# Performance work log

Measured on AMD Instinct MI355X. Metric: run time of the kernel, lower is better.

The kernel has to match this reference:

```python
import jax, jax.numpy as jnp
import numpy as np
import itertools

MAX_SRC_PER_MIX = 2
N_OUT = 2 * MAX_SRC_PER_MIX          # 4 estimated sources
N_COMB = 2 ** N_OUT                  # 16 assignment combinations
SNR_MAX = 30.0


def _a_tensor():
    # [16, 2, 4]: row 0 = combination mask, row 1 = its complement
    combos = np.array(list(itertools.product([0, 1], repeat=N_OUT)), dtype=np.float32)
    return jnp.asarray(np.stack([combos, 1.0 - combos], axis=1))


def setup_inputs() -> dict:
    key = jax.random.key(0)
    k1, k2, k3 = jax.random.split(key, 3)
    B, T = 32, 64000
    return {
        "estimated_sources": jax.random.normal(k1, (B, N_OUT, T), dtype=jnp.float32),
        "m1": jax.random.normal(k2, (B, T), dtype=jnp.float32),
        "m2": jax.random.normal(k3, (B, T), dtype=jnp.float32),
    }


def _snr_loss(y, y_pred):
    # y: [K, B, T] estimated mixture, y_pred: [1, B, T] reference mixture
    a = jnp.sum((y - y_pred) ** 2, axis=-1)   # [K, B]
    b = jnp.sum(y ** 2, axis=-1)              # [K, B]
    loss = 10.0 * jnp.log10(a + SNR_MAX * b) - 10.0 * jnp.log10(b)
    return jnp.sum(loss, axis=-1)             # [K]


def reference(estimated_sources, m1, m2):
    A = _a_tensor()                                              # [K, 2, S]
    # all combinations x batch in one contraction (contraction dim S=4)
    mix = jnp.einsum('kcs,bst->kbct', A, estimated_sources)      # [K, B, 2, T]
    losses = _snr_loss(mix[:, :, 0], m1[None]) + _snr_loss(mix[:, :, 1], m2[None])  # [K]
    return jnp.argmin(losses), jnp.min(losses)
```

## Files before the change

### kernel.cpp

```cpp
#include <hip/hip_runtime.h>
#include <math.h>

#define B      32
#define NSRC   4
#define T      64000
#define CH     64
#define NACC   20
#define KCOMB  16
#define NBLK   (B * CH)
#define TLEN4  ((T / CH) / 4)

#define DPP_QX1   0xB1
#define DPP_QX2   0x4E
#define DPP_HMIRR 0x141
#define DPP_MIRR  0x140

template <int CTRL>
__device__ __forceinline__ float dpp_add(float v) {
    int x = __builtin_amdgcn_update_dpp(0, __float_as_int(v), CTRL, 0xF, 0xF, true);
    return v + __int_as_float(x);
}

__device__ __forceinline__ void accum20(float* __restrict__ acc,
        const float4 v0, const float4 v1, const float4 v2, const float4 v3,
        const float4 w1, const float4 w2)
{
    const float A0[4] = {v0.x, v0.y, v0.z, v0.w};
    const float A1[4] = {v1.x, v1.y, v1.z, v1.w};
    const float A2[4] = {v2.x, v2.y, v2.z, v2.w};
    const float A3[4] = {v3.x, v3.y, v3.z, v3.w};
    const float M1[4] = {w1.x, w1.y, w1.z, w1.w};
    const float M2[4] = {w2.x, w2.y, w2.z, w2.w};
#pragma unroll
    for (int j = 0; j < 4; j++) {
        float s0 = A0[j], s1 = A1[j], s2 = A2[j], s3 = A3[j];
        float x = M1[j], y = M2[j];
        acc[0]  = fmaf(s0, s0, acc[0]);
        acc[1]  = fmaf(s0, s1, acc[1]);
        acc[2]  = fmaf(s0, s2, acc[2]);
        acc[3]  = fmaf(s0, s3, acc[3]);
        acc[4]  = fmaf(s1, s1, acc[4]);
        acc[5]  = fmaf(s1, s2, acc[5]);
        acc[6]  = fmaf(s1, s3, acc[6]);
        acc[7]  = fmaf(s2, s2, acc[7]);
        acc[8]  = fmaf(s2, s3, acc[8]);
        acc[9]  = fmaf(s3, s3, acc[9]);
        acc[10] = fmaf(s0, x,  acc[10]);
        acc[11] = fmaf(s1, x,  acc[11]);
        acc[12] = fmaf(s2, x,  acc[12]);
        acc[13] = fmaf(s3, x,  acc[13]);
        acc[14] = fmaf(s0, y,  acc[14]);
        acc[15] = fmaf(s1, y,  acc[15]);
        acc[16] = fmaf(s2, y,  acc[16]);
        acc[17] = fmaf(s3, y,  acc[17]);
        acc[18] = fmaf(x,  x,  acc[18]);
        acc[19] = fmaf(y,  y,  acc[19]);
    }
}

__global__ __launch_bounds__(256) void mixit_reduce_kernel(
    const float* __restrict__ est, const float* __restrict__ m1,
    const float* __restrict__ m2, float* __restrict__ ws)
{
    const int tid = threadIdx.x;
    const int b   = blockIdx.x / CH;
    const int ch  = blockIdx.x % CH;

    const float4* e0 = (const float4*)(est + (size_t)b * NSRC * T) + (size_t)ch * TLEN4;
    const float4* e1 = e0 + T / 4;
    const float4* e2 = e1 + T / 4;
    const float4* e3 = e2 + T / 4;
    const float4* p1 = (const float4*)(m1 + (size_t)b * T) + (size_t)ch * TLEN4;
    const float4* p2 = (const float4*)(m2 + (size_t)b * T) + (size_t)ch * TLEN4;

    float acc[NACC];
#pragma unroll
    for (int i = 0; i < NACC; i++) acc[i] = 0.0f;

    if (tid < TLEN4) {
        float4 v0 = e0[tid], v1 = e1[tid], v2 = e2[tid], v3 = e3[tid];
        float4 w1 = p1[tid], w2 = p2[tid];
        accum20(acc, v0, v1, v2, v3, w1, w2);
    }

#pragma unroll
    for (int a = 0; a < NACC; a++) {
        float v = acc[a];
        v = dpp_add<DPP_QX1>(v);
        v = dpp_add<DPP_QX2>(v);
        v = dpp_add<DPP_HMIRR>(v);
        v = dpp_add<DPP_MIRR>(v);
        int x = __builtin_amdgcn_ds_swizzle(__float_as_int(v), 0x401F);
        acc[a] = v + __int_as_float(x);
    }

    const int lane = tid & 63;
    const int wave = tid >> 6;
    __shared__ float red[8][NACC];
    if (lane == 0 || lane == 32) {
        const int r = wave * 2 + (lane >> 5);
#pragma unroll
        for (int a = 0; a < NACC; a++) red[r][a] = acc[a];
    }
    __syncthreads();
    if (tid < NACC) {
        float s = 0.0f;
#pragma unroll
        for (int r = 0; r < 8; r++) s += red[r][tid];
        ws[(size_t)tid * NBLK + blockIdx.x] = s;
    }
}

__global__ __launch_bounds__(1024) void mixit_finalize_kernel(
    const float* __restrict__ ws, float* __restrict__ out)
{
    __shared__ float sums[B * NACC];
    __shared__ float lkb[KCOMB * B];
    __shared__ float losses[KCOMB];

    const int t = threadIdx.x;

    if (t < B * NACC) {
        const int a  = t >> 5;
        const int bb = t & 31;
        const float4* p = (const float4*)(ws + (size_t)a * NBLK + bb * CH);
        float4 s4 = p[0];
#pragma unroll
        for (int i = 1; i < CH / 4; i++) {
            float4 q = p[i];
            s4.x += q.x; s4.y += q.y; s4.z += q.z; s4.w += q.w;
        }
        sums[bb * NACC + a] = (s4.x + s4.y) + (s4.z + s4.w);
    }
    __syncthreads();

    if (t < KCOMB * B) {
        const int k  = t >> 5;
        const int bb = t & 31;
        const float k0 = (float)((k >> 3) & 1);
        const float k1 = (float)((k >> 2) & 1);
        const float k2 = (float)((k >> 1) & 1);
        const float k3 = (float)(k & 1);
        const float u0 = 1.0f - k0, u1 = 1.0f - k1, u2 = 1.0f - k2, u3 = 1.0f - k3;

        const float* a = sums + bb * NACC;
        float g00 = a[0], g01 = a[1], g02 = a[2], g03 = a[3];
        float g11 = a[4], g12 = a[5], g13 = a[6];
        float g22 = a[7], g23 = a[8], g33 = a[9];

        float q0 = k0*k0*g00 + k1*k1*g11 + k2*k2*g22 + k3*k3*g33
                 + 2.0f*(k0*k1*g01 + k0*k2*g02 + k0*k3*g03
                       + k1*k2*g12 + k1*k3*g13 + k2*k3*g23);
        float q1 = u0*u0*g00 + u1*u1*g11 + u2*u2*g22 + u3*u3*g33
                 + 2.0f*(u0*u1*g01 + u0*u2*g02 + u0*u3*g03
                       + u1*u2*g12 + u1*u3*g13 + u2*u3*g23);
        float d1 = k0*a[10] + k1*a[11] + k2*a[12] + k3*a[13];
        float d2 = u0*a[14] + u1*a[15] + u2*a[16] + u3*a[17];

        float a0 = q0 - 2.0f*d1 + a[18];
        float a1 = q1 - 2.0f*d2 + a[19];

        float l = 10.0f * (log10f(fmaf(30.0f, q0, a0)) - log10f(q0))
                + 10.0f * (log10f(fmaf(30.0f, q1, a1)) - log10f(q1));
        lkb[k * B + bb] = l;
    }
    __syncthreads();

    if (t < KCOMB) {
        float s = 0.0f;
#pragma unroll
        for (int bb = 0; bb < B; bb++) s += lkb[t * B + bb];
        losses[t] = s;
    }
    __syncthreads();

    if (t == 0) {
        float best = losses[0];
        int bi = 0;
        for (int k = 1; k < KCOMB; k++)
            if (losses[k] < best) { best = losses[k]; bi = k; }
        out[0] = (float)bi;
        out[1] = best;
    }
}

extern "C" void kernel_launch(void* const* d_in, const int* in_sizes, int n_in,
                              void* d_out, int out_size, void* d_ws, size_t ws_size,
                              hipStream_t stream) {
    const float* est = (const float*)d_in[0];
    const float* m1  = (const float*)d_in[1];
    const float* m2  = (const float*)d_in[2];
    float* ws  = (float*)d_ws;
    float* out = (float*)d_out;

    mixit_reduce_kernel<<<NBLK, 256, 0, stream>>>(est, m1, m2, ws);
    mixit_finalize_kernel<<<1, 1024, 0, stream>>>(ws, out);
}
```

Baseline: 91.69 us.

## Fuse reduce and finalize into one kernel using atomics and last-block detection

Merges the two-kernel pipeline into a single launch. Each block atomically adds its 20 partial sums into a per-batch accumulator, and a global counter picks the last block to run the finalize (loss per combination plus argmin). This removes the second kernel launch and the strided workspace reread, at the cost of a memset before each call, 20 atomics per block, and a serialized tail in one block. Memory ordering relies on relaxed atomics with no explicit fence before the counter increment, so correctness depends on the hardware ordering those operations.

```diff
diff --git a/kernel.cpp b/kernel.cpp
--- a/kernel.cpp
+++ b/kernel.cpp
@@ -9,6 +9,8 @@
 #define KCOMB  16
 #define NBLK   (B * CH)
 #define TLEN4  ((T / CH) / 4)
+
+#define CNT_FLOAT_OFF 1024
 
 #define DPP_QX1   0xB1
 #define DPP_QX2   0x4E
@@ -58,9 +60,10 @@
     }
 }
 
-__global__ __launch_bounds__(256) void mixit_reduce_kernel(
+__global__ __launch_bounds__(256) void mixit_onekernel(
     const float* __restrict__ est, const float* __restrict__ m1,
-    const float* __restrict__ m2, float* __restrict__ ws)
+    const float* __restrict__ m2, float* __restrict__ ws,
+    float* __restrict__ out)
 {
     const int tid = threadIdx.x;
     const int b   = blockIdx.x / CH;
@@ -103,40 +106,39 @@
         for (int a = 0; a < NACC; a++) red[r][a] = acc[a];
     }
     __syncthreads();
+
     if (tid < NACC) {
         float s = 0.0f;
 #pragma unroll
         for (int r = 0; r < 8; r++) s += red[r][tid];
-        ws[(size_t)tid * NBLK + blockIdx.x] = s;
-    }
-}
-
-__global__ __launch_bounds__(1024) void mixit_finalize_kernel(
-    const float* __restrict__ ws, float* __restrict__ out)
-{
+        float old = atomicAdd(&ws[b * NACC + tid], s);
+        __asm__ volatile("" :: "v"(old));
+    }
+    __syncthreads();
+
+    __shared__ int isLast;
+    if (tid == 0) {
+        unsigned* cnt = (unsigned*)(ws + CNT_FLOAT_OFF);
+        unsigned t = __hip_atomic_fetch_add(cnt, 1u, __ATOMIC_RELAXED,
+                                            __HIP_MEMORY_SCOPE_AGENT);
+        isLast = (t == NBLK - 1) ? 1 : 0;
+    }
+    __syncthreads();
+    if (!isLast) return;
+
     __shared__ float sums[B * NACC];
+    for (int p = tid; p < B * NACC; p += 256) {
+        sums[p] = __hip_atomic_load(&ws[p], __ATOMIC_RELAXED,
+                                    __HIP_MEMORY_SCOPE_AGENT);
+    }
+    __syncthreads();
+
     __shared__ float lkb[KCOMB * B];
-    __shared__ float losses[KCOMB];
-
-    const int t = threadIdx.x;
-
-    if (t < B * NACC) {
-        const int a  = t >> 5;
-        const int bb = t & 31;
-        const float4* p = (const float4*)(ws + (size_t)a * NBLK + bb * CH);
-        float4 s4 = p[0];
-#pragma unroll
-        for (int i = 1; i < CH / 4; i++) {
-            float4 q = p[i];
-            s4.x += q.x; s4.y += q.y; s4.z += q.z; s4.w += q.w;
-        }
-        sums[bb * NACC + a] = (s4.x + s4.y) + (s4.z + s4.w);
-    }
-    __syncthreads();
-
-    if (t < KCOMB * B) {
-        const int k  = t >> 5;
-        const int bb = t & 31;
+#pragma unroll
+    for (int q = 0; q < 2; q++) {
+        const int t2 = tid + q * 256;
+        const int k  = t2 >> 5;
+        const int bb = t2 & 31;
         const float k0 = (float)((k >> 3) & 1);
         const float k1 = (float)((k >> 2) & 1);
         const float k2 = (float)((k >> 1) & 1);
@@ -160,21 +162,21 @@
         float a0 = q0 - 2.0f*d1 + a[18];
         float a1 = q1 - 2.0f*d2 + a[19];
 
-        float l = 10.0f * (log10f(fmaf(30.0f, q0, a0)) - log10f(q0))
-                + 10.0f * (log10f(fmaf(30.0f, q1, a1)) - log10f(q1));
-        lkb[k * B + bb] = l;
-    }
-    __syncthreads();
-
-    if (t < KCOMB) {
+        lkb[k * B + bb] = 10.0f * (log10f(fmaf(30.0f, q0, a0)) - log10f(q0))
+                        + 10.0f * (log10f(fmaf(30.0f, q1, a1)) - log10f(q1));
+    }
+    __syncthreads();
+
+    __shared__ float losses[KCOMB];
+    if (tid < KCOMB) {
         float s = 0.0f;
 #pragma unroll
-        for (int bb = 0; bb < B; bb++) s += lkb[t * B + bb];
-        losses[t] = s;
-    }
-    __syncthreads();
-
-    if (t == 0) {
+        for (int bb = 0; bb < B; bb++) s += lkb[tid * B + bb];
+        losses[tid] = s;
+    }
+    __syncthreads();
+
+    if (tid == 0) {
         float best = losses[0];
         int bi = 0;
         for (int k = 1; k < KCOMB; k++)
@@ -193,6 +195,6 @@
     float* ws  = (float*)d_ws;
     float* out = (float*)d_out;
 
-    mixit_reduce_kernel<<<NBLK, 256, 0, stream>>>(est, m1, m2, ws);
-    mixit_finalize_kernel<<<1, 1024, 0, stream>>>(ws, out);
-}
+    (void)hipMemsetAsync(d_ws, 0, 8192, stream);
+    mixit_onekernel<<<NBLK, 256, 0, stream>>>(est, m1, m2, ws, out);
+}
```

Result: slower. 107.7 us (+17.5%).
